# Kernel optimization log

Hardware: AMD Instinct MI355X
Metric: run time of the kernel (lower is better)

Reference implementation:

```python
import jax, jax.numpy as jnp
import numpy as np

B, S, HID = 1, 2048, 4096
NH, NKV, D = 32, 8, 128          # query heads, kv heads, head_dim
GROUPS = NH // NKV               # GQA repeat factor = 4
WINDOW = 1024                    # sliding-window size
ROPE_BASE = 10000.0


def setup_inputs() -> dict:
    key = jax.random.key(0)
    k = jax.random.split(key, 5)
    hidden_states = jax.random.normal(k[0], (B, S, HID), jnp.float32)
    Wq = jax.random.normal(k[1], (HID, HID), jnp.float32) * 0.02
    Wk = jax.random.normal(k[2], (NKV * D, HID), jnp.float32) * 0.02
    Wv = jax.random.normal(k[3], (NKV * D, HID), jnp.float32) * 0.02
    Wo = jax.random.normal(k[4], (HID, HID), jnp.float32) * 0.02
    position_ids = jnp.arange(S, dtype=jnp.int64 if jax.config.jax_enable_x64 else jnp.int32)[None, :]
    # Sliding-window causal additive mask [B,1,S,S]: key j visible to query i iff i-WINDOW < j <= i
    i = jnp.arange(S)
    visible = (i[None, :] <= i[:, None]) & (i[:, None] - i[None, :] < WINDOW)
    neg = jnp.finfo(jnp.float32).min
    attention_mask = jnp.where(visible, 0.0, neg)[None, None, :, :].astype(jnp.float32)
    return {"hidden_states": hidden_states, "attention_mask": attention_mask,
            "position_ids": position_ids, "Wq": Wq, "Wk": Wk, "Wv": Wv, "Wo": Wo}


def _rotate_half(x):
    x1, x2 = x[..., : D // 2], x[..., D // 2:]
    return jnp.concatenate((-x2, x1), axis=-1)


def _rope_cos_sin(position_ids, dtype):
    # inv_freq over even dims; gather-by-position_ids == direct indexing
    inv_freq = 1.0 / (ROPE_BASE ** (jnp.arange(0, D, 2, dtype=jnp.float32) / D))  # [D/2]
    freqs = position_ids.astype(jnp.float32)[..., None] * inv_freq                # [B,S,D/2]
    emb = jnp.concatenate((freqs, freqs), axis=-1)                                # [B,S,D]
    cos = jnp.cos(emb)[:, None, :, :].astype(dtype)                               # [B,1,S,D]
    sin = jnp.sin(emb)[:, None, :, :].astype(dtype)
    return cos, sin


def reference(hidden_states, attention_mask, position_ids, Wq, Wk, Wv, Wo):
    bsz, q_len, _ = hidden_states.shape
    # projections (nn.Linear: y = x @ W.T)
    q = (hidden_states @ Wq.T).reshape(bsz, q_len, NH, D).transpose(0, 2, 1, 3)    # [B,NH,S,D]
    k = (hidden_states @ Wk.T).reshape(bsz, q_len, NKV, D).transpose(0, 2, 1, 3)   # [B,NKV,S,D]
    v = (hidden_states @ Wv.T).reshape(bsz, q_len, NKV, D).transpose(0, 2, 1, 3)
    cos, sin = _rope_cos_sin(position_ids, q.dtype)
    q = q * cos + _rotate_half(q) * sin
    k = k * cos + _rotate_half(k) * sin
    # GQA repeat_kv (repeat_interleave along head dim)
    k = jnp.repeat(k, GROUPS, axis=1)                                              # [B,NH,S,D]
    v = jnp.repeat(v, GROUPS, axis=1)
    scores = jnp.einsum('bhqd,bhkd->bhqk', q, k) / np.sqrt(D)                       # [B,NH,S,S]
    scores = scores + attention_mask
    scores = jnp.maximum(scores, jnp.finfo(scores.dtype).min)
    probs = jax.nn.softmax(scores.astype(jnp.float32), axis=-1).astype(q.dtype)
    out = jnp.einsum('bhqk,bhkd->bhqd', probs, v)                                   # [B,NH,S,D]
    out = out.transpose(0, 2, 1, 3).reshape(bsz, q_len, HID)
    return out @ Wo.T
```

## Files before the change

### kernel.cpp

```cpp
#include <hip/hip_runtime.h>

#define S_LEN 2048
#define HID   4096
#define NH    32
#define NKV   8
#define DH    128
#define KVD   (NKV*DH)
#define WIN   1024
#define NTOT  6144

typedef __bf16 bf16_t;
typedef __bf16 bfrag  __attribute__((ext_vector_type(8)));
typedef __bf16 bf4    __attribute__((ext_vector_type(4)));
typedef float  ffrag  __attribute__((ext_vector_type(4)));
typedef float  f4     __attribute__((ext_vector_type(4)));

__global__ __launch_bounds__(256) void f32_to_bf16_kernel(const float* __restrict__ src,
                                                          bf16_t* __restrict__ dst, int n4) {
  int i = blockIdx.x * 256 + threadIdx.x;
  if (i < n4) {
    ffrag v = *(const ffrag*)(src + (size_t)i * 4);
    bf4 o;
    o[0] = (bf16_t)v[0]; o[1] = (bf16_t)v[1]; o[2] = (bf16_t)v[2]; o[3] = (bf16_t)v[3];
    *(bf4*)(dst + (size_t)i * 4) = o;
  }
}

__global__ __launch_bounds__(256) void cvt4_kernel(const float* __restrict__ h,
    const float* __restrict__ Wq, const float* __restrict__ Wk, const float* __restrict__ Wv,
    bf16_t* __restrict__ hB, bf16_t* __restrict__ WqB,
    bf16_t* __restrict__ WkB, bf16_t* __restrict__ WvB) {
  int i = blockIdx.x * 256 + threadIdx.x;
  const int N0 = S_LEN * HID / 4;
  const int N1 = N0 + HID * HID / 4;
  const int N2 = N1 + KVD * HID / 4;
  const float* s; bf16_t* d; int off;
  if (i < N0)      { s = h;  d = hB;  off = i; }
  else if (i < N1) { s = Wq; d = WqB; off = i - N0; }
  else if (i < N2) { s = Wk; d = WkB; off = i - N1; }
  else             { s = Wv; d = WvB; off = i - N2; }
  ffrag v = *(const ffrag*)(s + (size_t)off * 4);
  bf4 o;
  o[0] = (bf16_t)v[0]; o[1] = (bf16_t)v[1]; o[2] = (bf16_t)v[2]; o[3] = (bf16_t)v[3];
  *(bf4*)(d + (size_t)off * 4) = o;
}


__device__ __forceinline__ void load_lds16(const bf16_t* g, bf16_t* l) {
  __builtin_amdgcn_global_load_lds((__attribute__((address_space(1))) void*)g,
                                   (__attribute__((address_space(3))) void*)l,
                                   16, 0, 0);
}

#define BARW() asm volatile("s_barrier" ::: "memory")
#define WAITV(n) asm volatile("s_waitcnt vmcnt(" #n ")" ::: "memory")
#define LGKM0() do { asm volatile("s_waitcnt lgkmcnt(0)" ::: "memory"); \
                     __builtin_amdgcn_sched_barrier(0); } while (0)

template <int BN, int NT, int OUT_MODE>
__device__ __forceinline__ void gemm_body(const bf16_t* __restrict__ A,
                                          const bf16_t* __restrict__ B,
                                          void* __restrict__ Cv,
                                          int row0, int col0, int kbeg,
                                          int N, bf16_t* lds) {
  constexpr int K     = 4096;
  constexpr int WC    = BN / 4;
  constexpr int NTF   = WC / 16;
  constexpr int BSW   = BN / 64;
  constexpr int ABUFE = 256 * 64;
  constexpr int BBUFE = BN * 64;

  bf16_t* As0 = lds;
  bf16_t* Bs0 = lds + 2 * ABUFE;

  const int tid  = threadIdx.x;
  const int wave = tid >> 6;
  const int lane = tid & 63;
  const int wr = wave >> 2, wc = wave & 3;
  const int n = lane & 15, qd = lane >> 4;

  const int rsub = tid >> 3;
  const int sg   = (tid & 7) ^ (rsub & 7);
  const bf16_t* Ag = A + (size_t)(row0 + rsub) * K + sg * 8;
  const bf16_t* Bg = B + (size_t)(col0 + rsub) * K + sg * 8;
  const int wbase = wave * 512;

  const int pg0 = ( qd      ^ (n & 7)) * 8;
  const int pg1 = ((4 | qd) ^ (n & 7)) * 8;
  const int abase = (wr * 128 + n) * 64;
  const int bbase = (wc * WC + n) * 64;

  ffrag acc[8][NTF];
#pragma unroll
  for (int mt = 0; mt < 8; ++mt)
#pragma unroll
    for (int nt = 0; nt < NTF; ++nt) {
      acc[mt][nt][0] = 0.f; acc[mt][nt][1] = 0.f; acc[mt][nt][2] = 0.f; acc[mt][nt][3] = 0.f;
    }

  auto STAGE = [&](int t, int s) {
    const int ko = kbeg + t * 64;
    bf16_t* as = As0 + s * ABUFE + wbase;
    bf16_t* bs = Bs0 + s * BBUFE + wbase;
#pragma unroll
    for (int i = 0; i < 4; ++i)
      load_lds16(Ag + (size_t)(i * 64) * K + ko, as + i * 4096);
#pragma unroll
    for (int i = 0; i < BSW; ++i)
      load_lds16(Bg + (size_t)(i * 64) * K + ko, bs + i * 4096);
  };

  STAGE(0, 0); STAGE(1, 1);
  if constexpr (BN == 192) { WAITV(7); } else { WAITV(8); }
  BARW();

  for (int t = 0; t < NT; ++t) {
    const int s = t & 1;
    const bf16_t* Asl = As0 + s * ABUFE;
    const bf16_t* Bsl = Bs0 + s * BBUFE;
    bfrag av[8], bv[NTF];

#pragma unroll
    for (int mt = 0; mt < 8; ++mt) av[mt] = *(const bfrag*)(Asl + abase + mt * 1024 + pg0);
#pragma unroll
    for (int nt = 0; nt < NTF; ++nt) bv[nt] = *(const bfrag*)(Bsl + bbase + nt * 1024 + pg0);
    __builtin_amdgcn_s_setprio(1);
#pragma unroll
    for (int mt = 0; mt < 8; ++mt)
#pragma unroll
      for (int nt = 0; nt < NTF; ++nt)
        acc[mt][nt] = __builtin_amdgcn_mfma_f32_16x16x32_bf16(av[mt], bv[nt], acc[mt][nt], 0, 0, 0);
    __builtin_amdgcn_s_setprio(0);

#pragma unroll
    for (int mt = 0; mt < 8; ++mt) av[mt] = *(const bfrag*)(Asl + abase + mt * 1024 + pg1);
#pragma unroll
    for (int nt = 0; nt < NTF; ++nt) bv[nt] = *(const bfrag*)(Bsl + bbase + nt * 1024 + pg1);
    __builtin_amdgcn_s_setprio(1);
#pragma unroll
    for (int mt = 0; mt < 8; ++mt)
#pragma unroll
      for (int nt = 0; nt < NTF; ++nt)
        acc[mt][nt] = __builtin_amdgcn_mfma_f32_16x16x32_bf16(av[mt], bv[nt], acc[mt][nt], 0, 0, 0);
    __builtin_amdgcn_s_setprio(0);

    LGKM0();
    BARW();
    if (t + 2 < NT) STAGE(t + 2, s);
    if (t + 1 < NT) {
      if (t + 2 < NT) { if constexpr (BN == 192) { WAITV(7); } else { WAITV(8); } }
      else            { WAITV(0); }
      BARW();
    }
  }

  const int orow = row0 + wr * 128 + qd * 4;
  const int ocol = col0 + wc * WC + n;
#pragma unroll
  for (int mt = 0; mt < 8; ++mt)
#pragma unroll
    for (int nt = 0; nt < NTF; ++nt)
#pragma unroll
      for (int r = 0; r < 4; ++r) {
        size_t idx = (size_t)(orow + mt * 16 + r) * N + (ocol + nt * 16);
        if (OUT_MODE == 1) ((bf16_t*)Cv)[idx] = (bf16_t)acc[mt][nt][r];
        else               atomicAdd(&((float*)Cv)[idx], acc[mt][nt][r]);
      }
}

__global__ __launch_bounds__(512, 2) void gemm_qkv_kernel(const bf16_t* __restrict__ hB,
                                                          const bf16_t* __restrict__ Wqkv,
                                                          bf16_t* __restrict__ C) {
  __shared__ __align__(16) bf16_t lds[2 * 256 * 64 + 2 * 192 * 64];
  const int raw  = blockIdx.x;
  const int xcd  = raw & 7;
  const int slot = raw >> 3;
  const int bx   = xcd * 4 + (slot & 3);
  const int by   = slot >> 2;
  gemm_body<192, 64, 1>(hB, Wqkv, C, by * 256, bx * 192, 0, NTOT, lds);
}

__global__ __launch_bounds__(512, 2) void gemm_out_kernel(const bf16_t* __restrict__ A,
                                                          const bf16_t* __restrict__ B,
                                                          float* __restrict__ out) {
  __shared__ __align__(16) bf16_t lds[2 * 256 * 64 + 2 * 256 * 64];
  const int raw  = blockIdx.x;
  const int xcd  = raw & 7;
  const int slot = raw >> 3;
  const int bx   = xcd * 2 + (slot & 1);
  const int by   = (slot >> 1) & 7;
  const int kz   = slot >> 4;
  gemm_body<256, 32, 2>(A, B, out, by * 256, bx * 256, kz * 2048, HID, lds);
}

__global__ __launch_bounds__(256) void ropecvt_kernel(const bf16_t* __restrict__ Cqkv,
                                                      bf16_t* __restrict__ Qb,
                                                      bf16_t* __restrict__ Kb,
                                                      bf16_t* __restrict__ Vb) {
  int idx = blockIdx.x * 256 + threadIdx.x;
  int g  = idx & 7;
  int t  = idx >> 3;
  int hh = t % 48;
  int s  = t / 48;
  const bf16_t* r0 = Cqkv + (size_t)s * NTOT + hh * 128;
  bfrag a0 = *(const bfrag*)&r0[g * 8];
  bfrag a1 = *(const bfrag*)&r0[g * 8 + 64];
  bf16_t* p;
  bool rope;
  if (hh < NH)           { p = Qb + (size_t)s * HID + hh * DH;        rope = true; }
  else if (hh < NH+NKV)  { p = Kb + (size_t)s * KVD + (hh - NH) * DH; rope = true; }
  else                   { p = Vb + (size_t)s * KVD + (hh - 40) * DH; rope = false; }
  bfrag o1, o2;
#pragma unroll
  for (int j = 0; j < 8; ++j) {
    float x1 = (float)a0[j];
    float x2 = (float)a1[j];
    if (rope) {
      int d = g * 8 + j;
      float inv = exp2f((float)d * (-13.287712379549449f / 64.f));
      float ang = (float)s * inv;
      float sn = sinf(ang), cs = cosf(ang);
      o1[j] = (bf16_t)(x1 * cs - x2 * sn);
      o2[j] = (bf16_t)(x2 * cs + x1 * sn);
    } else {
      o1[j] = (bf16_t)x1;
      o2[j] = (bf16_t)x2;
    }
  }
  *(bfrag*)&p[g * 8]      = o1;
  *(bfrag*)&p[g * 8 + 64] = o2;
}

#define KS_STRIDE 136
#define VT_STRIDE 72
#define PS_STRIDE 72

__global__ __launch_bounds__(256, 3) void attn_kernel(const bf16_t* __restrict__ Q,
                                                      const bf16_t* __restrict__ Kc,
                                                      const bf16_t* __restrict__ Vc,
                                                      bf16_t* __restrict__ AO) {
  const int qt   = 31 - blockIdx.x;
  const int h    = blockIdx.y;
  const int kvh  = h >> 2;
  const int q0   = qt * 64;
  const int tid  = threadIdx.x;
  const int wq   = tid >> 6;
  const int lane = tid & 63;
  const int n    = lane & 15;
  const int quad = lane >> 4;
  const float scale = 0.08838834764831845f;

  __shared__ __align__(16) bf16_t Ks[64 * KS_STRIDE];
  __shared__ __align__(16) bf16_t VT[128 * VT_STRIDE];
  __shared__ __align__(16) bf16_t Ps[4][16 * PS_STRIDE];

  bfrag aq[4];
#pragma unroll
  for (int kc = 0; kc < 4; ++kc) {
    bfrag t = *(const bfrag*)&Q[(size_t)(q0 + wq * 16 + n) * HID + h * DH + kc * 32 + quad * 8];
#pragma unroll
    for (int e = 0; e < 8; ++e) t[e] = (bf16_t)((float)t[e] * scale);
    aq[kc] = t;
  }

  ffrag acc[8];
#pragma unroll
  for (int dt = 0; dt < 8; ++dt) { acc[dt][0] = 0.f; acc[dt][1] = 0.f; acc[dt][2] = 0.f; acc[dt][3] = 0.f; }
  float lrow[4] = {0.f, 0.f, 0.f, 0.f};

  const int ktlo = (q0 >= WIN) ? ((q0 - (WIN - 1)) >> 6) : 0;
  const int kthi = (q0 + 63) >> 6;

  const int kg = tid & 15;
  const int dg = tid >> 4;

  bfrag pk[4], pv[4];
  {
    const int k0 = ktlo * 64;
#pragma unroll
    for (int i = 0; i < 4; ++i) {
      int pos = i * 256 + tid;
      pk[i] = *(const bfrag*)&Kc[(size_t)(k0 + (pos >> 4)) * KVD + kvh * DH + (pos & 15) * 8];
    }
#pragma unroll
    for (int j = 0; j < 4; ++j)
      pv[j] = *(const bfrag*)&Vc[(size_t)(k0 + j * 16 + kg) * KVD + kvh * DH + dg * 8];
  }

  for (int kt = ktlo; kt <= kthi; ++kt) {
    const int k0 = kt * 64;
    __syncthreads();
#pragma unroll
    for (int i = 0; i < 4; ++i) {
      int pos = i * 256 + tid;
      *(bfrag*)&Ks[(pos >> 4) * KS_STRIDE + (pos & 15) * 8] = pk[i];
    }
#pragma unroll
    for (int i = 0; i < 8; ++i) {
      bf4 pkk;
      pkk[0] = pv[0][i]; pkk[1] = pv[1][i]; pkk[2] = pv[2][i]; pkk[3] = pv[3][i];
      *(bf4*)&VT[(dg * 8 + i) * VT_STRIDE + kg * 4] = pkk;
    }
    __syncthreads();
    if (kt < kthi) {
      const int k1 = k0 + 64;
#pragma unroll
      for (int i = 0; i < 4; ++i) {
        int pos = i * 256 + tid;
        pk[i] = *(const bfrag*)&Kc[(size_t)(k1 + (pos >> 4)) * KVD + kvh * DH + (pos & 15) * 8];
      }
#pragma unroll
      for (int j = 0; j < 4; ++j)
        pv[j] = *(const bfrag*)&Vc[(size_t)(k1 + j * 16 + kg) * KVD + kvh * DH + dg * 8];
    }

    ffrag s[4];
#pragma unroll
    for (int nt = 0; nt < 4; ++nt) { s[nt][0] = 0.f; s[nt][1] = 0.f; s[nt][2] = 0.f; s[nt][3] = 0.f; }
#pragma unroll
    for (int kc = 0; kc < 4; ++kc) {
      bfrag bk[4];
#pragma unroll
      for (int nt = 0; nt < 4; ++nt)
        bk[nt] = *(const bfrag*)&Ks[(nt * 16 + n) * KS_STRIDE + kc * 32 + quad * 8];
#pragma unroll
      for (int nt = 0; nt < 4; ++nt)
        s[nt] = __builtin_amdgcn_mfma_f32_16x16x32_bf16(aq[kc], bk[nt], s[nt], 0, 0, 0);
    }

    const bool full = (k0 + 63 <= q0) && (q0 + 63 - k0 < WIN);
    if (!full) {
#pragma unroll
      for (int nt = 0; nt < 4; ++nt)
#pragma unroll
        for (int r = 0; r < 4; ++r) {
          int q = q0 + wq * 16 + quad * 4 + r;
          int k = k0 + nt * 16 + n;
          bool vis = (k <= q) && ((q - k) < WIN);
          if (!vis) s[nt][r] = -1e30f;
        }
    }

#pragma unroll
    for (int r = 0; r < 4; ++r) {
      bf4 pkk;
      float ps0 = __expf(s[0][r]);
      float ps1 = __expf(s[1][r]);
      float ps2 = __expf(s[2][r]);
      float ps3 = __expf(s[3][r]);
      lrow[r] += (ps0 + ps1) + (ps2 + ps3);
      pkk[0] = (bf16_t)ps0; pkk[1] = (bf16_t)ps1; pkk[2] = (bf16_t)ps2; pkk[3] = (bf16_t)ps3;
      *(bf4*)&Ps[wq][(quad * 4 + r) * PS_STRIDE + n * 4] = pkk;
    }

#pragma unroll
    for (int kc = 0; kc < 2; ++kc) {
      bfrag ap = *(const bfrag*)&Ps[wq][n * PS_STRIDE + kc * 32 + quad * 8];
#pragma unroll
      for (int dt = 0; dt < 8; ++dt) {
        bfrag bv = *(const bfrag*)&VT[(dt * 16 + n) * VT_STRIDE + kc * 32 + quad * 8];
        acc[dt] = __builtin_amdgcn_mfma_f32_16x16x32_bf16(ap, bv, acc[dt], 0, 0, 0);
      }
    }
  }

#pragma unroll
  for (int off = 1; off < 16; off <<= 1)
#pragma unroll
    for (int r = 0; r < 4; ++r) lrow[r] += __shfl_xor(lrow[r], off);
  float inv[4];
#pragma unroll
  for (int r = 0; r < 4; ++r) inv[r] = 1.f / lrow[r];
#pragma unroll
  for (int dt = 0; dt < 8; ++dt)
#pragma unroll
    for (int r = 0; r < 4; ++r)
      AO[(size_t)(q0 + wq * 16 + quad * 4 + r) * HID + h * DH + dt * 16 + n] =
          (bf16_t)(acc[dt][r] * inv[r]);
}

extern "C" void kernel_launch(void* const* d_in, const int* in_sizes, int n_in,
                              void* d_out, int out_size, void* d_ws, size_t ws_size,
                              hipStream_t stream) {
  const float* h  = (const float*)d_in[0];
  const float* Wq = (const float*)d_in[3];
  const float* Wk = (const float*)d_in[4];
  const float* Wv = (const float*)d_in[5];
  const float* Wo = (const float*)d_in[6];
  float* out = (float*)d_out;

  char* ws = (char*)d_ws;
  const size_t MB = (size_t)1 << 20;
  bf16_t* hB    = (bf16_t*)(ws + 0 * MB);
  bf16_t* Qb    = (bf16_t*)(ws + 0 * MB);
  bf16_t* WqB   = (bf16_t*)(ws + 16 * MB);
  bf16_t* WkB   = (bf16_t*)(ws + 48 * MB);
  bf16_t* WvB   = (bf16_t*)(ws + 56 * MB);
  bf16_t* Cqkv  = (bf16_t*)(ws + 64 * MB);
  bf16_t* WoB   = (bf16_t*)(ws + 64 * MB);
  bf16_t* AOb   = (bf16_t*)(ws + 96 * MB);
  bf16_t* Kb    = (bf16_t*)(ws + 112 * MB);
  bf16_t* Vb    = (bf16_t*)(ws + 116 * MB);

  cvt4_kernel<<<(S_LEN * HID + HID * HID + 2 * KVD * HID) / 4 / 256, 256, 0, stream>>>(
      h, Wq, Wk, Wv, hB, WqB, WkB, WvB);

  gemm_qkv_kernel<<<256, 512, 0, stream>>>(hB, WqB, Cqkv);

  ropecvt_kernel<<<(S_LEN * 48 * 8) / 256, 256, 0, stream>>>(Cqkv, Qb, Kb, Vb);

  f32_to_bf16_kernel<<<(HID * HID / 4 + 255) / 256, 256, 0, stream>>>(Wo, WoB, HID * HID / 4);

  attn_kernel<<<dim3(32, NH), 256, 0, stream>>>(Qb, Kb, Vb, AOb);

  hipMemsetAsync(out, 0, (size_t)S_LEN * HID * sizeof(float), stream);

  gemm_out_kernel<<<256, 512, 0, stream>>>(AOb, WoB, out);
}
```

Measured before the change: 493.8 us.

## Shrink GEMM N-tile to 64, drop split-K atomics, add MFMA priority in attention

```diff
diff --git a/kernel.cpp b/kernel.cpp
--- a/kernel.cpp
+++ b/kernel.cpp
@@ -57,18 +57,16 @@
 #define LGKM0() do { asm volatile("s_waitcnt lgkmcnt(0)" ::: "memory"); \
                      __builtin_amdgcn_sched_barrier(0); } while (0)
 
-template <int BN, int NT, int OUT_MODE>
+template <int OUT_MODE>
 __device__ __forceinline__ void gemm_body(const bf16_t* __restrict__ A,
                                           const bf16_t* __restrict__ B,
                                           void* __restrict__ Cv,
-                                          int row0, int col0, int kbeg,
+                                          int row0, int col0,
                                           int N, bf16_t* lds) {
   constexpr int K     = 4096;
-  constexpr int WC    = BN / 4;
-  constexpr int NTF   = WC / 16;
-  constexpr int BSW   = BN / 64;
+  constexpr int NT    = K / 64;
   constexpr int ABUFE = 256 * 64;
-  constexpr int BBUFE = BN * 64;
+  constexpr int BBUFE = 64 * 64;
 
   bf16_t* As0 = lds;
   bf16_t* Bs0 = lds + 2 * ABUFE;
@@ -87,110 +85,96 @@
 
   const int pg0 = ( qd      ^ (n & 7)) * 8;
   const int pg1 = ((4 | qd) ^ (n & 7)) * 8;
-  const int abase = (wr * 128 + n) * 64;
-  const int bbase = (wc * WC + n) * 64;
-
-  ffrag acc[8][NTF];
-#pragma unroll
-  for (int mt = 0; mt < 8; ++mt)
-#pragma unroll
-    for (int nt = 0; nt < NTF; ++nt) {
-      acc[mt][nt][0] = 0.f; acc[mt][nt][1] = 0.f; acc[mt][nt][2] = 0.f; acc[mt][nt][3] = 0.f;
-    }
+  const int abase = wr * 8192 + n * 64;
+  const int bbase = wc * 1024 + n * 64;
+
+  ffrag acc[8];
+#pragma unroll
+  for (int mt = 0; mt < 8; ++mt) {
+    acc[mt][0] = 0.f; acc[mt][1] = 0.f; acc[mt][2] = 0.f; acc[mt][3] = 0.f;
+  }
 
   auto STAGE = [&](int t, int s) {
-    const int ko = kbeg + t * 64;
+    const int ko = t * 64;
     bf16_t* as = As0 + s * ABUFE + wbase;
-    bf16_t* bs = Bs0 + s * BBUFE + wbase;
 #pragma unroll
     for (int i = 0; i < 4; ++i)
       load_lds16(Ag + (size_t)(i * 64) * K + ko, as + i * 4096);
-#pragma unroll
-    for (int i = 0; i < BSW; ++i)
-      load_lds16(Bg + (size_t)(i * 64) * K + ko, bs + i * 4096);
+    load_lds16(Bg + ko, Bs0 + s * BBUFE + wbase);
   };
 
   STAGE(0, 0); STAGE(1, 1);
-  if constexpr (BN == 192) { WAITV(7); } else { WAITV(8); }
+  WAITV(5);
   BARW();
 
   for (int t = 0; t < NT; ++t) {
     const int s = t & 1;
     const bf16_t* Asl = As0 + s * ABUFE;
     const bf16_t* Bsl = Bs0 + s * BBUFE;
-    bfrag av[8], bv[NTF];
+    bfrag av[8], bv;
 
 #pragma unroll
     for (int mt = 0; mt < 8; ++mt) av[mt] = *(const bfrag*)(Asl + abase + mt * 1024 + pg0);
-#pragma unroll
-    for (int nt = 0; nt < NTF; ++nt) bv[nt] = *(const bfrag*)(Bsl + bbase + nt * 1024 + pg0);
+    bv = *(const bfrag*)(Bsl + bbase + pg0);
     __builtin_amdgcn_s_setprio(1);
 #pragma unroll
     for (int mt = 0; mt < 8; ++mt)
-#pragma unroll
-      for (int nt = 0; nt < NTF; ++nt)
-        acc[mt][nt] = __builtin_amdgcn_mfma_f32_16x16x32_bf16(av[mt], bv[nt], acc[mt][nt], 0, 0, 0);
+      acc[mt] = __builtin_amdgcn_mfma_f32_16x16x32_bf16(av[mt], bv, acc[mt], 0, 0, 0);
     __builtin_amdgcn_s_setprio(0);
 
 #pragma unroll
     for (int mt = 0; mt < 8; ++mt) av[mt] = *(const bfrag*)(Asl + abase + mt * 1024 + pg1);
-#pragma unroll
-    for (int nt = 0; nt < NTF; ++nt) bv[nt] = *(const bfrag*)(Bsl + bbase + nt * 1024 + pg1);
+    bv = *(const bfrag*)(Bsl + bbase + pg1);
     __builtin_amdgcn_s_setprio(1);
 #pragma unroll
     for (int mt = 0; mt < 8; ++mt)
-#pragma unroll
-      for (int nt = 0; nt < NTF; ++nt)
-        acc[mt][nt] = __builtin_amdgcn_mfma_f32_16x16x32_bf16(av[mt], bv[nt], acc[mt][nt], 0, 0, 0);
+      acc[mt] = __builtin_amdgcn_mfma_f32_16x16x32_bf16(av[mt], bv, acc[mt], 0, 0, 0);
     __builtin_amdgcn_s_setprio(0);
 
     LGKM0();
     BARW();
     if (t + 2 < NT) STAGE(t + 2, s);
     if (t + 1 < NT) {
-      if (t + 2 < NT) { if constexpr (BN == 192) { WAITV(7); } else { WAITV(8); } }
+      if (t + 2 < NT) { WAITV(5); }
       else            { WAITV(0); }
       BARW();
     }
   }
 
   const int orow = row0 + wr * 128 + qd * 4;
-  const int ocol = col0 + wc * WC + n;
+  const int ocol = col0 + wc * 16 + n;
 #pragma unroll
   for (int mt = 0; mt < 8; ++mt)
 #pragma unroll
-    for (int nt = 0; nt < NTF; ++nt)
-#pragma unroll
-      for (int r = 0; r < 4; ++r) {
-        size_t idx = (size_t)(orow + mt * 16 + r) * N + (ocol + nt * 16);
-        if (OUT_MODE == 1) ((bf16_t*)Cv)[idx] = (bf16_t)acc[mt][nt][r];
-        else               atomicAdd(&((float*)Cv)[idx], acc[mt][nt][r]);
-      }
-}
-
-__global__ __launch_bounds__(512, 2) void gemm_qkv_kernel(const bf16_t* __restrict__ hB,
+    for (int r = 0; r < 4; ++r) {
+      size_t idx = (size_t)(orow + mt * 16 + r) * N + ocol;
+      if (OUT_MODE == 1) ((bf16_t*)Cv)[idx] = (bf16_t)acc[mt][r];
+      else               ((float*)Cv)[idx]  = acc[mt][r];
+    }
+}
+
+__global__ __launch_bounds__(512, 4) void gemm_qkv_kernel(const bf16_t* __restrict__ hB,
                                                           const bf16_t* __restrict__ Wqkv,
                                                           bf16_t* __restrict__ C) {
-  __shared__ __align__(16) bf16_t lds[2 * 256 * 64 + 2 * 192 * 64];
+  __shared__ __align__(16) bf16_t lds[2 * 256 * 64 + 2 * 64 * 64];
   const int raw  = blockIdx.x;
   const int xcd  = raw & 7;
   const int slot = raw >> 3;
-  const int bx   = xcd * 4 + (slot & 3);
-  const int by   = slot >> 2;
-  gemm_body<192, 64, 1>(hB, Wqkv, C, by * 256, bx * 192, 0, NTOT, lds);
-}
-
-__global__ __launch_bounds__(512, 2) void gemm_out_kernel(const bf16_t* __restrict__ A,
+  const int bx   = xcd * 12 + slot % 12;
+  const int by   = slot / 12;
+  gemm_body<1>(hB, Wqkv, C, by * 256, bx * 64, NTOT, lds);
+}
+
+__global__ __launch_bounds__(512, 4) void gemm_out_kernel(const bf16_t* __restrict__ A,
                                                           const bf16_t* __restrict__ B,
                                                           float* __restrict__ out) {
-  __shared__ __align__(16) bf16_t lds[2 * 256 * 64 + 2 * 256 * 64];
+  __shared__ __align__(16) bf16_t lds[2 * 256 * 64 + 2 * 64 * 64];
   const int raw  = blockIdx.x;
   const int xcd  = raw & 7;
   const int slot = raw >> 3;
-  const int bx   = xcd * 2 + (slot & 1);
-  const int by   = (slot >> 1) & 7;
-  const int kz   = slot >> 4;
-  gemm_body<256, 32, 2>(A, B, out, by * 256, bx * 256, kz * 2048, HID, lds);
+  const int bx   = xcd * 8 + (slot & 7);
+  const int by   = slot >> 3;
+  gemm_body<0>(A, B, out, by * 256, bx * 64, HID, lds);
 }
 
 __global__ __launch_bounds__(256) void ropecvt_kernel(const bf16_t* __restrict__ Cqkv,
@@ -323,9 +307,11 @@
 #pragma unroll
       for (int nt = 0; nt < 4; ++nt)
         bk[nt] = *(const bfrag*)&Ks[(nt * 16 + n) * KS_STRIDE + kc * 32 + quad * 8];
+      __builtin_amdgcn_s_setprio(1);
 #pragma unroll
       for (int nt = 0; nt < 4; ++nt)
         s[nt] = __builtin_amdgcn_mfma_f32_16x16x32_bf16(aq[kc], bk[nt], s[nt], 0, 0, 0);
+      __builtin_amdgcn_s_setprio(0);
     }
 
     const bool full = (k0 + 63 <= q0) && (q0 + 63 - k0 < WIN);
@@ -357,9 +343,17 @@
     for (int kc = 0; kc < 2; ++kc) {
       bfrag ap = *(const bfrag*)&Ps[wq][n * PS_STRIDE + kc * 32 + quad * 8];
 #pragma unroll
-      for (int dt = 0; dt < 8; ++dt) {
-        bfrag bv = *(const bfrag*)&VT[(dt * 16 + n) * VT_STRIDE + kc * 32 + quad * 8];
-        acc[dt] = __builtin_amdgcn_mfma_f32_16x16x32_bf16(ap, bv, acc[dt], 0, 0, 0);
+      for (int dt = 0; dt < 8; dt += 4) {
+        bfrag bv0 = *(const bfrag*)&VT[((dt + 0) * 16 + n) * VT_STRIDE + kc * 32 + quad * 8];
+        bfrag bv1 = *(const bfrag*)&VT[((dt + 1) * 16 + n) * VT_STRIDE + kc * 32 + quad * 8];
+        bfrag bv2 = *(const bfrag*)&VT[((dt + 2) * 16 + n) * VT_STRIDE + kc * 32 + quad * 8];
+        bfrag bv3 = *(const bfrag*)&VT[((dt + 3) * 16 + n) * VT_STRIDE + kc * 32 + quad * 8];
+        __builtin_amdgcn_s_setprio(1);
+        acc[dt + 0] = __builtin_amdgcn_mfma_f32_16x16x32_bf16(ap, bv0, acc[dt + 0], 0, 0, 0);
+        acc[dt + 1] = __builtin_amdgcn_mfma_f32_16x16x32_bf16(ap, bv1, acc[dt + 1], 0, 0, 0);
+        acc[dt + 2] = __builtin_amdgcn_mfma_f32_16x16x32_bf16(ap, bv2, acc[dt + 2], 0, 0, 0);
+        acc[dt + 3] = __builtin_amdgcn_mfma_f32_16x16x32_bf16(ap, bv3, acc[dt + 3], 0, 0, 0);
+        __builtin_amdgcn_s_setprio(0);
       }
     }
   }
@@ -405,7 +399,7 @@
   cvt4_kernel<<<(S_LEN * HID + HID * HID + 2 * KVD * HID) / 4 / 256, 256, 0, stream>>>(
       h, Wq, Wk, Wv, hB, WqB, WkB, WvB);
 
-  gemm_qkv_kernel<<<256, 512, 0, stream>>>(hB, WqB, Cqkv);
+  gemm_qkv_kernel<<<768, 512, 0, stream>>>(hB, WqB, Cqkv);
 
   ropecvt_kernel<<<(S_LEN * 48 * 8) / 256, 256, 0, stream>>>(Cqkv, Qb, Kb, Vb);
 
@@ -413,7 +407,5 @@
 
   attn_kernel<<<dim3(32, NH), 256, 0, stream>>>(Qb, Kb, Vb, AOb);
 
-  hipMemsetAsync(out, 0, (size_t)S_LEN * HID * sizeof(float), stream);
-
-  gemm_out_kernel<<<256, 512, 0, stream>>>(AOb, WoB, out);
-}
+  gemm_out_kernel<<<512, 512, 0, stream>>>(AOb, WoB, out);
+}
```

Result: faster. 464.7 us (-5.9%).
